# Kernel tuning notes

Measured on AMD Instinct MI355X. Metric: run time of the kernel, lower is better.

The kernel has to match this reference:

```python
import jax, jax.numpy as jnp
from jax import lax
import numpy as np

LRELU_SLOPE = 0.2
DEMOD_EPS = 1e-8


def _mod_conv(x, style, weight, bias, demodulate, pad):
    """StyleGAN2 modulated conv via grouped conv (groups = batch).
    x: [B,Cin,H,W]; style: [B,Cin]; weight: [Cout,Cin,kh,kw]; bias: [Cout]."""
    B, Cin, H, W = x.shape
    Cout, _, kh, kw = weight.shape
    # per-sample modulated weight [B,Cout,Cin,kh,kw]
    wt = weight[None] * style[:, None, :, None, None]
    if demodulate:
        wt = wt / jnp.sqrt(jnp.sum(wt ** 2, axis=(2, 3, 4), keepdims=True) + DEMOD_EPS)
    out = lax.conv_general_dilated(
        x.reshape(1, B * Cin, H, W),
        wt.reshape(B * Cout, Cin, kh, kw),
        window_strides=(1, 1),
        padding=[(pad, pad), (pad, pad)],
        dimension_numbers=('NCHW', 'OIHW', 'NCHW'),
        feature_group_count=B,
    )
    return out.reshape(B, Cout, H, W) + bias[None, :, None, None]


def setup_inputs() -> dict:
    key = jax.random.key(0)
    ks = jax.random.split(key, 16)
    B, Cin, Cout, Wd, H = 4, 512, 256, 512, 64
    f32 = jnp.float32
    d = {
        'x': jax.random.normal(ks[0], (B, Cin, H, H), f32),
        'w': jax.random.normal(ks[1], (B, Wd), f32),
        # conv1: Cin->Cout 3x3
        'w1': jax.random.normal(ks[2], (Cout, Cin, 3, 3), f32) / np.float32(np.sqrt(Cin * 9)),
        'b1': jax.random.normal(ks[3], (Cout,), f32) * 0.01,
        'a1w': jax.random.normal(ks[4], (Cin, Wd), f32) / np.float32(np.sqrt(Wd)),
        'a1b': jnp.ones((Cin,), f32),
        # conv2: Cout->Cout 3x3
        'w2': jax.random.normal(ks[5], (Cout, Cout, 3, 3), f32) / np.float32(np.sqrt(Cout * 9)),
        'b2': jax.random.normal(ks[6], (Cout,), f32) * 0.01,
        'a2w': jax.random.normal(ks[7], (Cout, Wd), f32) / np.float32(np.sqrt(Wd)),
        'a2b': jnp.ones((Cout,), f32),
        # to_rgb: Cout->3 1x1, no demodulation
        'w3': jax.random.normal(ks[8], (3, Cout, 1, 1), f32) / np.float32(np.sqrt(Cout)),
        'b3': jax.random.normal(ks[9], (3,), f32) * 0.01,
        'a3w': jax.random.normal(ks[10], (Cout, Wd), f32) / np.float32(np.sqrt(Wd)),
        'a3b': jnp.ones((Cout,), f32),
    }
    return d


def reference(x, w, w1, b1, a1w, a1b, w2, b2, a2w, a2b, w3, b3, a3w, a3b):
    B, C, H, W = x.shape
    # nn.Upsample(scale_factor=2, mode='bilinear', align_corners=False) == half-pixel bilinear
    xu = jax.image.resize(x, (B, C, 2 * H, 2 * W), method='bilinear')
    s1 = w @ a1w.T + a1b                      # affine -> per-sample style [B,Cin]
    h = jax.nn.leaky_relu(_mod_conv(xu, s1, w1, b1, True, 1), LRELU_SLOPE)
    s2 = w @ a2w.T + a2b
    h = jax.nn.leaky_relu(_mod_conv(h, s2, w2, b2, True, 1), LRELU_SLOPE)
    s3 = w @ a3w.T + a3b
    rgb = jax.nn.leaky_relu(_mod_conv(h, s3, w3, b3, False, 0), LRELU_SLOPE)
    return (h, rgb)
```

## Files before the change

### kernel.cpp

```cpp
#include <hip/hip_runtime.h>
#include <stdint.h>

typedef __attribute__((ext_vector_type(8))) short bhalf8;
typedef __attribute__((ext_vector_type(4))) float fx4;

__device__ __forceinline__ unsigned short f2bf(float f) {
    unsigned u = __builtin_bit_cast(unsigned, f);
    unsigned r = (u + 0x7fffu + ((u >> 16) & 1u)) >> 16;
    return (unsigned short)r;
}
__device__ __forceinline__ float bf2f(unsigned short h) {
    unsigned u = ((unsigned)h) << 16;
    return __builtin_bit_cast(float, u);
}
__device__ __forceinline__ float lrelu(float v) { return v > 0.f ? v : 0.2f * v; }

typedef __attribute__((address_space(1))) void as1_void;
typedef __attribute__((address_space(3))) void as3_void;
__device__ __forceinline__ void gl_lds16(const void* g, void* l) {
    __builtin_amdgcn_global_load_lds((as1_void*)(void*)g, (as3_void*)l, 16, 0, 0);
}

__global__ __launch_bounds__(256) void style_kernel(
    const float* __restrict__ w,
    const float* __restrict__ a1w, const float* __restrict__ a1b,
    const float* __restrict__ a2w, const float* __restrict__ a2b,
    const float* __restrict__ a3w, const float* __restrict__ a3b,
    float* __restrict__ s1, float* __restrict__ s2, float* __restrict__ s3)
{
    int gw = blockIdx.x * 4 + (threadIdx.x >> 6);
    int lane = threadIdx.x & 63;
    int b = gw >> 10, r = gw & 1023;
    const float* arow; const float* abias; float* dst;
    if (r < 512)      { arow = a1w + (size_t)r * 512;        abias = a1b + r;       dst = s1 + b * 512 + r; }
    else if (r < 768) { int rr = r - 512; arow = a2w + (size_t)rr * 512; abias = a2b + rr; dst = s2 + b * 256 + rr; }
    else              { int rr = r - 768; arow = a3w + (size_t)rr * 512; abias = a3b + rr; dst = s3 + b * 256 + rr; }
    const float* wrow = w + b * 512;
    float acc = 0.f;
    #pragma unroll
    for (int j = 0; j < 8; ++j) {
        int c = lane + j * 64;
        acc += wrow[c] * arow[c];
    }
    #pragma unroll
    for (int off = 32; off; off >>= 1) acc += __shfl_down(acc, off, 64);
    if (lane == 0) *dst = acc + *abias;
}

__global__ __launch_bounds__(256) void demod_kernel(
    const float* __restrict__ w1, const float* __restrict__ w2,
    const float* __restrict__ s1, const float* __restrict__ s2,
    float* __restrict__ d1, float* __restrict__ d2)
{
    int blk = blockIdx.x;
    int conv = blk >> 10, b = (blk >> 8) & 3, o = blk & 255;
    int t = threadIdx.x;
    int cin = conv ? 256 : 512;
    const float* s = conv ? (s2 + b * 256) : (s1 + b * 512);
    const float* row = (conv ? w2 : w1) + (size_t)o * cin * 9;
    __shared__ float sv[512];
    for (int i = t; i < cin; i += 256) { float v = s[i]; sv[i] = v * v; }
    __syncthreads();
    float sum = 0.f;
    int n = cin * 9;
    for (int k = t; k < n; k += 256) {
        float v = row[k];
        sum += v * v * sv[k / 9];
    }
    #pragma unroll
    for (int off = 32; off; off >>= 1) sum += __shfl_down(sum, off, 64);
    __shared__ float red[4];
    if ((t & 63) == 0) red[t >> 6] = sum;
    __syncthreads();
    if (t == 0) {
        float tot = red[0] + red[1] + red[2] + red[3];
        (conv ? d2 : d1)[b * 256 + o] = rsqrtf(tot + 1e-8f);
    }
}

__global__ __launch_bounds__(256) void pack_kernel(
    const float* __restrict__ w1, const float* __restrict__ w2,
    unsigned short* __restrict__ wp1, unsigned short* __restrict__ wp2)
{
    int tid = blockIdx.x * 256 + threadIdx.x;
    const int N1 = 1179648, N2 = 589824;
    if (tid < N1) {
        int e = tid & 7, m = (tid >> 3) & 127, kh = (tid >> 10) & 3;
        int dx = (tid >> 12) % 3, ic = (tid / 12288) & 15;
        int dy = (tid / 196608) % 3, mblk = tid / 589824;
        int o = mblk * 128 + m, ci = ic * 32 + kh * 8 + e;
        wp1[tid] = f2bf(w1[((size_t)o * 512 + ci) * 9 + dy * 3 + dx]);
    } else if (tid < N1 + N2) {
        int t2 = tid - N1;
        int e = t2 & 7, m = (t2 >> 3) & 127, kh = (t2 >> 10) & 3;
        int dx = (t2 >> 12) % 3, ic = (t2 / 12288) & 7;
        int dy = (t2 / 98304) % 3, mblk = t2 / 294912;
        int o = mblk * 128 + m, ci = ic * 32 + kh * 8 + e;
        wp2[t2] = f2bf(w2[((size_t)o * 256 + ci) * 9 + dy * 3 + dx]);
    }
}

__global__ __launch_bounds__(256) void upsample_kernel(
    const float* __restrict__ x, const float* __restrict__ s1,
    unsigned short* __restrict__ xu)
{
    __shared__ float L[2][64][65];
    int bid = blockIdx.x, t = threadIdx.x;
    int yo = bid & 127, b = bid >> 7;
    int k = yo >> 1;
    int sy0, sy1; float wy0, wy1;
    if ((yo & 1) == 0) { sy0 = k > 0 ? k - 1 : 0; sy1 = k; wy0 = 0.25f; wy1 = 0.75f; }
    else               { sy0 = k; sy1 = k < 63 ? k + 1 : 63; wy0 = 0.75f; wy1 = 0.25f; }
    for (int c0 = 0; c0 < 512; c0 += 64) {
        __syncthreads();
        #pragma unroll
        for (int j = 0; j < 32; ++j) {
            int f = t + j * 256;
            int idx = f & 63, rowid = f >> 6;
            int cc = rowid & 63, which = rowid >> 6;
            int sy = which ? sy1 : sy0;
            L[which][cc][idx] = x[((size_t)(b * 512 + c0 + cc) * 64 + sy) * 64 + idx];
        }
        __syncthreads();
        #pragma unroll
        for (int j = 0; j < 16; ++j) {
            int it = t + j * 256;
            int cp = it & 31, xo = it >> 5;
            int kk = xo >> 1, sx0, sx1; float wx0, wx1;
            if ((xo & 1) == 0) { sx0 = kk > 0 ? kk - 1 : 0; sx1 = kk; wx0 = 0.25f; wx1 = 0.75f; }
            else               { sx0 = kk; sx1 = kk < 63 ? kk + 1 : 63; wx0 = 0.75f; wx1 = 0.25f; }
            int c = cp * 2;
            float A0 = wx0 * L[0][c][sx0] + wx1 * L[0][c][sx1];
            float B0 = wx0 * L[1][c][sx0] + wx1 * L[1][c][sx1];
            float A1 = wx0 * L[0][c + 1][sx0] + wx1 * L[0][c + 1][sx1];
            float B1 = wx0 * L[1][c + 1][sx0] + wx1 * L[1][c + 1][sx1];
            float v0 = (wy0 * A0 + wy1 * B0) * s1[b * 512 + c0 + c];
            float v1 = (wy0 * A1 + wy1 * B1) * s1[b * 512 + c0 + c + 1];
            unsigned pk = (unsigned)f2bf(v0) | ((unsigned)f2bf(v1) << 16);
            *(unsigned*)&xu[((size_t)(b * 128 + yo) * 128 + xo) * 512 + c0 + c] = pk;
        }
    }
}

template<int CIN, bool IS_CONV2>
__global__ __launch_bounds__(256) void conv3x3_kernel(
    const unsigned short* __restrict__ inp,
    const unsigned short* __restrict__ wpack,
    const float* __restrict__ dvec,
    const float* __restrict__ bias,
    const float* __restrict__ post,
    unsigned short* __restrict__ outmod,
    float* __restrict__ outf)
{
    constexpr int NIC = CIN / 32;
    __shared__ __attribute__((aligned(16))) short Alds[3 * 4096];
    __shared__ __attribute__((aligned(16))) short Blds[130 * 32];
    const int tid = threadIdx.x;
    const int lane = tid & 63;
    const int wvi = tid >> 6;
    const int bid = blockIdx.x;
    const int y = bid & 127;
    const int mblk = (bid >> 7) & 1;
    const int b = bid >> 8;
    const int wm = (wvi >> 1) * 64;
    const int wn = (wvi & 1) * 64;
    const int lhi = lane >> 4;
    const int llo = lane & 15;

    if (tid < 8) {
        int s = (tid >= 4) ? 129 : 0;
        *(int4*)((char*)Blds + s * 64 + (tid & 3) * 16) = make_int4(0, 0, 0, 0);
    }

    fx4 acc[4][4];
    #pragma unroll
    for (int mt = 0; mt < 4; ++mt)
        #pragma unroll
        for (int nt = 0; nt < 4; ++nt) acc[mt][nt] = (fx4){0.f, 0.f, 0.f, 0.f};

    for (int dy = 0; dy < 3; ++dy) {
        const int yy = y + dy - 1;
        const bool inrow = ((unsigned)yy < 128u);
        const unsigned short* brow = inp + ((size_t)(b * 128 + yy) * 128) * CIN;
        for (int ic = 0; ic < NIC; ++ic) {
            __syncthreads();
            const unsigned short* asrc = wpack + ((size_t)((mblk * 3 + dy) * NIC + ic)) * (3 * 4096);
            #pragma unroll
            for (int j = 0; j < 6; ++j) {
                int g = tid + j * 256;
                gl_lds16(asrc + (size_t)g * 8, (char*)Alds + g * 16);
            }
            if (inrow) {
                #pragma unroll
                for (int j = 0; j < 2; ++j) {
                    int g = tid + j * 256;
                    int xg = g >> 2, i8 = g & 3;
                    int i8s = i8 ^ ((xg >> 1) & 3);
                    gl_lds16(brow + (size_t)xg * CIN + ic * 32 + i8s * 8,
                             (char*)Blds + 64 + g * 16);
                }
            } else {
                #pragma unroll
                for (int j = 0; j < 2; ++j) {
                    int g = tid + j * 256;
                    *(int4*)((char*)Blds + 64 + g * 16) = make_int4(0, 0, 0, 0);
                }
            }
            __syncthreads();
            #pragma unroll
            for (int dx = 0; dx < 3; ++dx) {
                bhalf8 af[4], bfr[4];
                #pragma unroll
                for (int mt = 0; mt < 4; ++mt)
                    af[mt] = *(const bhalf8*)&Alds[dx * 4096 + (lhi * 128 + wm + mt * 16 + llo) * 8];
                #pragma unroll
                for (int nt = 0; nt < 4; ++nt) {
                    int s = wn + nt * 16 + llo + dx;
                    int key = ((s - 1) >> 1) & 3;
                    bfr[nt] = *(const bhalf8*)&Blds[s * 32 + ((lhi ^ key) << 3)];
                }
                #pragma unroll
                for (int mt = 0; mt < 4; ++mt)
                    #pragma unroll
                    for (int nt = 0; nt < 4; ++nt)
                        acc[mt][nt] = __builtin_amdgcn_mfma_f32_16x16x32_bf16(
                            af[mt], bfr[nt], acc[mt][nt], 0, 0, 0);
            }
        }
    }

    #pragma unroll
    for (int mt = 0; mt < 4; ++mt) {
        const int o0 = mblk * 128 + wm + mt * 16 + lhi * 4;
        const fx4 d4 = *(const fx4*)(dvec + b * 256 + o0);
        const fx4 bb4 = *(const fx4*)(bias + o0);
        const fx4 p4 = *(const fx4*)(post + b * 256 + o0);
        #pragma unroll
        for (int nt = 0; nt < 4; ++nt) {
            const int xo = wn + nt * 16 + llo;
            unsigned lo = 0, hi = 0;
            #pragma unroll
            for (int r = 0; r < 4; ++r) {
                float v = acc[mt][nt][r] * d4[r] + bb4[r];
                v = lrelu(v);
                if (IS_CONV2)
                    outf[(((size_t)b * 256 + o0 + r) * 128 + y) * 128 + xo] = v;
                unsigned short ub = f2bf(v * p4[r]);
                if (r < 2) lo |= (unsigned)ub << (16 * r);
                else       hi |= (unsigned)ub << (16 * (r - 2));
            }
            *(uint2*)&outmod[((size_t)(b * 128 + y) * 128 + xo) * 256 + o0] = make_uint2(lo, hi);
        }
    }
}

__global__ __launch_bounds__(256) void rgb_kernel(
    const unsigned short* __restrict__ hs3,
    const float* __restrict__ w3, const float* __restrict__ b3,
    float* __restrict__ out)
{
    __shared__ float wl[768];
    int t = threadIdx.x;
    for (int i = t; i < 768; i += 256) wl[i] = w3[i];
    __syncthreads();
    int p = blockIdx.x * 64 + (t >> 2);
    int q = t & 3;
    const unsigned short* src = hs3 + (size_t)p * 256 + q * 64;
    float a0 = 0.f, a1 = 0.f, a2 = 0.f;
    #pragma unroll
    for (int c8 = 0; c8 < 64; c8 += 8) {
        int4 pk = *(const int4*)(src + c8);
        #pragma unroll
        for (int qq = 0; qq < 4; ++qq) {
            unsigned uu = ((const unsigned*)&pk)[qq];
            float ve = bf2f((unsigned short)(uu & 0xffffu));
            float vo = bf2f((unsigned short)(uu >> 16));
            int c = q * 64 + c8 + qq * 2;
            a0 += ve * wl[c] + vo * wl[c + 1];
            a1 += ve * wl[256 + c] + vo * wl[256 + c + 1];
            a2 += ve * wl[512 + c] + vo * wl[512 + c + 1];
        }
    }
    a0 += __shfl_xor(a0, 1, 64); a0 += __shfl_xor(a0, 2, 64);
    a1 += __shfl_xor(a1, 1, 64); a1 += __shfl_xor(a1, 2, 64);
    a2 += __shfl_xor(a2, 1, 64); a2 += __shfl_xor(a2, 2, 64);
    int b = p >> 14, yx = p & 16383;
    if (q < 3) {
        float v = (q == 0) ? a0 : (q == 1) ? a1 : a2;
        out[((size_t)b * 3 + q) * 16384 + yx] = lrelu(v + b3[q]);
    }
}

extern "C" void kernel_launch(void* const* d_in, const int* in_sizes, int n_in,
                              void* d_out, int out_size, void* d_ws, size_t ws_size,
                              hipStream_t stream) {
    const float* x   = (const float*)d_in[0];
    const float* w   = (const float*)d_in[1];
    const float* w1  = (const float*)d_in[2];
    const float* b1  = (const float*)d_in[3];
    const float* a1w = (const float*)d_in[4];
    const float* a1b = (const float*)d_in[5];
    const float* w2  = (const float*)d_in[6];
    const float* b2  = (const float*)d_in[7];
    const float* a2w = (const float*)d_in[8];
    const float* a2b = (const float*)d_in[9];
    const float* w3  = (const float*)d_in[10];
    const float* b3  = (const float*)d_in[11];
    const float* a3w = (const float*)d_in[12];
    const float* a3b = (const float*)d_in[13];

    char* ws = (char*)d_ws;
    unsigned short* xu  = (unsigned short*)(ws);
    unsigned short* hs3 = (unsigned short*)(ws);
    unsigned short* t1  = (unsigned short*)(ws + 67108864);
    unsigned short* wp1 = (unsigned short*)(ws + 100663296);
    unsigned short* wp2 = (unsigned short*)(ws + 103022592);
    float* s1 = (float*)(ws + 104202240);
    float* s2 = (float*)(ws + 104210432);
    float* s3 = (float*)(ws + 104214528);
    float* d1 = (float*)(ws + 104218624);
    float* d2 = (float*)(ws + 104222720);

    float* h_out   = (float*)d_out;
    float* rgb_out = h_out + 16777216;

    style_kernel<<<1024, 256, 0, stream>>>(w, a1w, a1b, a2w, a2b, a3w, a3b, s1, s2, s3);
    demod_kernel<<<2048, 256, 0, stream>>>(w1, w2, s1, s2, d1, d2);
    pack_kernel<<<6912, 256, 0, stream>>>(w1, w2, wp1, wp2);
    upsample_kernel<<<512, 256, 0, stream>>>(x, s1, xu);
    conv3x3_kernel<512, false><<<1024, 256, 0, stream>>>(xu, wp1, d1, b1, s2, t1, nullptr);
    conv3x3_kernel<256, true><<<1024, 256, 0, stream>>>(t1, wp2, d2, b2, s3, hs3, h_out);
    rgb_kernel<<<1024, 256, 0, stream>>>(hs3, w3, b3, rgb_out);
}
```

Measured before the change: 391.7 us.

## Compute two output rows per conv block to reuse weight tiles across rows

Each conv3x3 block now has 512 threads and computes two output rows instead of one. It stages four input rows in LDS per input-channel chunk, and each weight tile per dy is loaded once and shared by both rows' waves. This halves global weight traffic and the input-row reloads across dy. In exchange it adds extra barriers per dy step, uses more LDS for the four row buffers, and halves the grid to 512 blocks. That lowers the number of blocks available to spread across the CUs.

```diff
diff --git a/kernel.cpp b/kernel.cpp
--- a/kernel.cpp
+++ b/kernel.cpp
@@ -143,7 +143,7 @@
 }
 
 template<int CIN, bool IS_CONV2>
-__global__ __launch_bounds__(256) void conv3x3_kernel(
+__global__ __launch_bounds__(512, 4) void conv3x3_kernel(
     const unsigned short* __restrict__ inp,
     const unsigned short* __restrict__ wpack,
     const float* __restrict__ dvec,
@@ -154,22 +154,23 @@
 {
     constexpr int NIC = CIN / 32;
     __shared__ __attribute__((aligned(16))) short Alds[3 * 4096];
-    __shared__ __attribute__((aligned(16))) short Blds[130 * 32];
+    __shared__ __attribute__((aligned(16))) short Blds[4][4160];
     const int tid = threadIdx.x;
     const int lane = tid & 63;
     const int wvi = tid >> 6;
     const int bid = blockIdx.x;
-    const int y = bid & 127;
-    const int mblk = (bid >> 7) & 1;
-    const int b = bid >> 8;
-    const int wm = (wvi >> 1) * 64;
+    const int y0 = (bid & 63) << 1;
+    const int mblk = (bid >> 6) & 1;
+    const int b = bid >> 7;
+    const int wm = (wvi >> 2) * 64;
+    const int row = (wvi >> 1) & 1;
     const int wn = (wvi & 1) * 64;
     const int lhi = lane >> 4;
     const int llo = lane & 15;
 
-    if (tid < 8) {
-        int s = (tid >= 4) ? 129 : 0;
-        *(int4*)((char*)Blds + s * 64 + (tid & 3) * 16) = make_int4(0, 0, 0, 0);
+    if (tid < 32) {
+        int buf = tid >> 3, slot = ((tid >> 2) & 1) ? 129 : 0, part = tid & 3;
+        *(int4*)((char*)&Blds[buf][0] + slot * 64 + part * 16) = make_int4(0, 0, 0, 0);
     }
 
     fx4 acc[4][4];
@@ -178,35 +179,33 @@
         #pragma unroll
         for (int nt = 0; nt < 4; ++nt) acc[mt][nt] = (fx4){0.f, 0.f, 0.f, 0.f};
 
-    for (int dy = 0; dy < 3; ++dy) {
-        const int yy = y + dy - 1;
-        const bool inrow = ((unsigned)yy < 128u);
-        const unsigned short* brow = inp + ((size_t)(b * 128 + yy) * 128) * CIN;
-        for (int ic = 0; ic < NIC; ++ic) {
-            __syncthreads();
-            const unsigned short* asrc = wpack + ((size_t)((mblk * 3 + dy) * NIC + ic)) * (3 * 4096);
+    for (int ic = 0; ic < NIC; ++ic) {
+        {
+            const int xg = tid >> 2, i8 = tid & 3;
+            const int i8s = i8 ^ ((xg >> 1) & 3);
             #pragma unroll
-            for (int j = 0; j < 6; ++j) {
-                int g = tid + j * 256;
+            for (int rr = 0; rr < 4; ++rr) {
+                const int yy = y0 - 1 + rr;
+                char* dstB = (char*)&Blds[rr][0] + 64 + tid * 16;
+                if ((unsigned)yy < 128u) {
+                    gl_lds16(inp + ((size_t)(b * 128 + yy) * 128 + xg) * CIN + ic * 32 + i8s * 8, dstB);
+                } else {
+                    *(int4*)dstB = make_int4(0, 0, 0, 0);
+                }
+            }
+        }
+        {
+            const unsigned short* asrc = wpack + ((size_t)(mblk * 3 + 0) * NIC + ic) * 12288;
+            #pragma unroll
+            for (int j = 0; j < 3; ++j) {
+                int g = tid + j * 512;
                 gl_lds16(asrc + (size_t)g * 8, (char*)Alds + g * 16);
             }
-            if (inrow) {
-                #pragma unroll
-                for (int j = 0; j < 2; ++j) {
-                    int g = tid + j * 256;
-                    int xg = g >> 2, i8 = g & 3;
-                    int i8s = i8 ^ ((xg >> 1) & 3);
-                    gl_lds16(brow + (size_t)xg * CIN + ic * 32 + i8s * 8,
-                             (char*)Blds + 64 + g * 16);
-                }
-            } else {
-                #pragma unroll
-                for (int j = 0; j < 2; ++j) {
-                    int g = tid + j * 256;
-                    *(int4*)((char*)Blds + 64 + g * 16) = make_int4(0, 0, 0, 0);
-                }
-            }
-            __syncthreads();
+        }
+        __syncthreads();
+        #pragma unroll
+        for (int dy = 0; dy < 3; ++dy) {
+            const short* Brow = &Blds[row + dy][0];
             #pragma unroll
             for (int dx = 0; dx < 3; ++dx) {
                 bhalf8 af[4], bfr[4];
@@ -217,7 +216,7 @@
                 for (int nt = 0; nt < 4; ++nt) {
                     int s = wn + nt * 16 + llo + dx;
                     int key = ((s - 1) >> 1) & 3;
-                    bfr[nt] = *(const bhalf8*)&Blds[s * 32 + ((lhi ^ key) << 3)];
+                    bfr[nt] = *(const bhalf8*)&Brow[s * 32 + ((lhi ^ key) << 3)];
                 }
                 #pragma unroll
                 for (int mt = 0; mt < 4; ++mt)
@@ -226,9 +225,20 @@
                         acc[mt][nt] = __builtin_amdgcn_mfma_f32_16x16x32_bf16(
                             af[mt], bfr[nt], acc[mt][nt], 0, 0, 0);
             }
-        }
-    }
-
+            __syncthreads();
+            if (dy < 2) {
+                const unsigned short* asrc = wpack + ((size_t)(mblk * 3 + dy + 1) * NIC + ic) * 12288;
+                #pragma unroll
+                for (int j = 0; j < 3; ++j) {
+                    int g = tid + j * 512;
+                    gl_lds16(asrc + (size_t)g * 8, (char*)Alds + g * 16);
+                }
+                __syncthreads();
+            }
+        }
+    }
+
+    const int y = y0 + row;
     #pragma unroll
     for (int mt = 0; mt < 4; ++mt) {
         const int o0 = mblk * 128 + wm + mt * 16 + lhi * 4;
@@ -328,7 +338,7 @@
     demod_kernel<<<2048, 256, 0, stream>>>(w1, w2, s1, s2, d1, d2);
     pack_kernel<<<6912, 256, 0, stream>>>(w1, w2, wp1, wp2);
     upsample_kernel<<<512, 256, 0, stream>>>(x, s1, xu);
-    conv3x3_kernel<512, false><<<1024, 256, 0, stream>>>(xu, wp1, d1, b1, s2, t1, nullptr);
-    conv3x3_kernel<256, true><<<1024, 256, 0, stream>>>(t1, wp2, d2, b2, s3, hs3, h_out);
+    conv3x3_kernel<512, false><<<512, 512, 0, stream>>>(xu, wp1, d1, b1, s2, t1, nullptr);
+    conv3x3_kernel<256, true><<<512, 512, 0, stream>>>(t1, wp2, d2, b2, s3, hs3, h_out);
     rgb_kernel<<<1024, 256, 0, stream>>>(hs3, w3, b3, rgb_out);
 }
```

After: 381.0 us. -2.7%, faster.
